# Kernel optimization log

Measured on AMD Instinct MI355X. Metric: run time of the kernel, lower is better.

Reference implementation:

```python
import jax, jax.numpy as jnp
import numpy as np

RES = 3.5
K = (np.pi / RES) ** 2          # Gaussian falloff constant
BW2 = 6.0                        # squared neighborhood radius (voxels)
R = 3                            # floor(idx - sqrt(6)) = idx-3, ceil(idx + sqrt(6)) = idx+3


def _offsets():
    o = jnp.arange(-R, R + 1)
    oz, oy, ox = jnp.meshgrid(o, o, o, indexing='ij')
    offs = jnp.stack([oz.ravel(), oy.ravel(), ox.ravel()], axis=-1)  # (343, 3)
    d2 = jnp.sum(offs * offs, axis=-1)                               # (343,)
    return offs, d2


def _splat(coords, x0, y0, z0, vox, G):
    """coords: (N,3) atom positions. Returns (G,G,G) density grid via scatter-max."""
    idx = jnp.stack([
        jnp.floor((coords[:, 0] - x0[0]) / vox[0]),
        jnp.floor((coords[:, 1] - y0[0]) / vox[0]),
        jnp.floor((coords[:, 2] - z0[0]) / vox[0]),
    ], axis=1).astype(jnp.int32)                                     # (N, 3)

    offs, d2 = _offsets()
    pos = idx[:, None, :] + offs[None, :, :]                         # (N, 343, 3)

    M = G - 1                                                        # min(dims) - 1 (cubic grid)
    lc = jnp.clip(idx - R, 0, M)                                     # clamped bbox lower (N,3)
    uc = jnp.clip(idx + R, 0, M)                                     # clamped bbox upper (N,3)
    in_range = jnp.all((pos >= lc[:, None, :]) & (pos <= uc[:, None, :]), axis=-1)
    center_ok = jnp.all((idx >= 0) & (idx < G), axis=-1)             # atom's own voxel inside grid
    valid = in_range & (d2 <= BW2)[None, :] & center_ok[:, None]     # (N, 343)

    prob = jnp.where(valid, jnp.exp(-K * d2.astype(jnp.float32))[None, :], 0.0)

    pos_c = jnp.clip(pos, 0, G - 1)                                  # safe indices for invalid slots
    flat = (pos_c[..., 0] * G + pos_c[..., 1]) * G + pos_c[..., 2]   # (N, 343)

    grid = jnp.zeros((G * G * G,), dtype=jnp.float32)
    grid = grid.at[flat.reshape(-1)].max(prob.reshape(-1))           # scatter-max (grid init 0, prob >= 0)
    return grid.reshape(G, G, G)


def setup_inputs() -> dict:
    key = jax.random.key(0)
    k1, k2 = jax.random.split(key)
    G = 256
    N = 20000
    src = jax.random.uniform(k1, (1, 3, N), dtype=jnp.float32, minval=0.0, maxval=float(G))
    tgt = jax.random.uniform(k2, (1, 3, N), dtype=jnp.float32, minval=0.0, maxval=float(G))
    return {
        'src': src,
        'tgt': tgt,
        'x_origin': jnp.zeros((1,), jnp.float32),
        'y_origin': jnp.zeros((1,), jnp.float32),
        'z_origin': jnp.zeros((1,), jnp.float32),
        'x_voxel': jnp.ones((1,), jnp.float32),
        'grid_dim': G,
    }


def reference(src, tgt, x_origin, y_origin, z_origin, x_voxel, grid_dim):
    G = int(grid_dim)
    src_c = src[0].T                                                 # (N, 3)
    tgt_c = tgt[0].T
    src_mask = _splat(src_c, x_origin, y_origin, z_origin, x_voxel, G)
    tgt_mask = _splat(tgt_c, x_origin, y_origin, z_origin, x_voxel, G)
    # global_alignment_loss: tgt <- tgt*src ; src <- src*src ; loss = mean(sum(src) - sum(tgt))
    rho_em = jnp.sum(tgt_mask * src_mask)
    rho_mo = jnp.sum(src_mask * src_mask)
    return rho_mo - rho_em
```

## Files before the change

### kernel.cpp

```cpp
#include <hip/hip_runtime.h>

#define GDIM   256
#define NCOLS  1024
#define CAP    128
#define NQ     2048

__global__ void bin_kernel(const float* __restrict__ src,
                           const float* __restrict__ tgt,
                           const float* __restrict__ ox,
                           const float* __restrict__ oy,
                           const float* __restrict__ oz,
                           const float* __restrict__ vox,
                           unsigned* __restrict__ cnt,
                           unsigned* __restrict__ entries,
                           float* __restrict__ out,
                           int N)
{
    int a = blockIdx.x * blockDim.x + threadIdx.x;
    int m = blockIdx.y;
    if (a == 0 && m == 0) *out = 0.0f;
    if (a >= N) return;

    const float* c = m ? tgt : src;
    float vx = vox[0];
    int i0 = (int)floorf((c[a]         - ox[0]) / vx);
    int i1 = (int)floorf((c[N + a]     - oy[0]) / vx);
    int i2 = (int)floorf((c[2 * N + a] - oz[0]) / vx);
    if ((unsigned)i0 >= GDIM || (unsigned)i1 >= GDIM || (unsigned)i2 >= GDIM) return;

    unsigned pk = (unsigned)i0 | ((unsigned)i1 << 8) | ((unsigned)i2 << 16);
    int tlx = max(i0 - 2, 0) >> 4, thx = min(i0 + 2, GDIM - 1) >> 4;
    int tly = max(i1 - 2, 0) >> 4, thy = min(i1 + 2, GDIM - 1) >> 4;
    int tlz = max(i2 - 2, 0) >> 6, thz = min(i2 + 2, GDIM - 1) >> 6;

    for (int tx = tlx; tx <= thx; ++tx)
        for (int ty = tly; ty <= thy; ++ty)
            for (int tz = tlz; tz <= thz; ++tz) {
                int bin = m * NCOLS + (((tx << 4) + ty) << 2) + tz;
                unsigned slot = atomicAdd(&cnt[bin], 1u);
                if (slot < CAP) entries[bin * CAP + slot] = pk;
            }
}

__global__ __launch_bounds__(256, 4)
void tile_kernel(const unsigned* __restrict__ cnt,
                 const unsigned* __restrict__ entries,
                 float* __restrict__ out)
{
    __shared__ unsigned long long smem[2 * NQ];
    __shared__ unsigned eS[CAP], eT[CAP];
    __shared__ float tblp[49];
    __shared__ float wsum[4];

    constexpr int OX[21] = {-2,-2,-2,-1,-1,-1,-1,-1, 0, 0, 0, 0, 0, 1, 1, 1, 1, 1, 2, 2, 2};
    constexpr int OY[21] = {-1, 0, 1,-2,-1, 0, 1, 2,-2,-1, 0, 1, 2,-2,-1, 0, 1, 2,-1, 0, 1};
    constexpr unsigned long long PATC[21] = {
        0x0040204000ull, 0x0020102000ull, 0x0040204000ull,
        0x0040204000ull, 0x4008040840ull, 0x2004020420ull, 0x4008040840ull, 0x0040204000ull,
        0x0020102000ull, 0x2004020420ull, 0x1002010210ull, 0x2004020420ull, 0x0020102000ull,
        0x0040204000ull, 0x4008040840ull, 0x2004020420ull, 0x4008040840ull, 0x0040204000ull,
        0x0040204000ull, 0x0020102000ull, 0x0040204000ull,
    };

    int tid = threadIdx.x;
    int t   = blockIdx.x;
    int cx0 = (t >> 6) << 4;
    int cy0 = ((t >> 2) & 15) << 4;
    int cz0 = (t & 3) << 6;

    const float kf = (float)((3.14159265358979323846 / 3.5) * (3.14159265358979323846 / 3.5));
    if (tid < 49) {
        int a = tid / 7, b = tid - 7 * a;
        tblp[tid] = expf(-kf * (float)a) * expf(-kf * (float)b);
    }
    {
        uint4* zp = (uint4*)smem;
        #pragma unroll
        for (int i = 0; i < 8; ++i) zp[tid + i * 256] = make_uint4(0u, 0u, 0u, 0u);
    }
    int nS = min(cnt[t],         (unsigned)CAP);
    int nT = min(cnt[NCOLS + t], (unsigned)CAP);
    if (tid < nS) eS[tid] = entries[t * CAP + tid];
    if (tid < nT) eT[tid] = entries[(NCOLS + t) * CAP + tid];
    __syncthreads();

#define SPLAT_R(r) {                                                              \
        int l0 = x0 + OX[r];                                                      \
        int l1 = y0 + OY[r];                                                      \
        if ((unsigned)l0 < 16u && (unsigned)l1 < 16u) {                           \
            unsigned long long pat = (PATC[r] >> (8 * drop)) & kmask;             \
            if (pat) {                                                            \
                unsigned long long* q = base + (((l0 << 10) | (l1 << 6) | zb) >> 3); \
                unsigned long long lo = pat << (8 * off);                         \
                if (lo) atomicOr(q, lo);                                          \
                if (spill) {                                                      \
                    unsigned long long hi = pat >> (8 * (8 - off));               \
                    if (hi) atomicOr(q + 1, hi);                                  \
                }                                                                 \
            }                                                                     \
        }                                                                         \
    }
    {
        int lane = tid & 63, wv = tid >> 6;
        int nTot = nS + nT;
        for (int e = lane; e < nTot; e += 64) {
            int m        = e >= nS;
            unsigned pk  = m ? eT[e - nS] : eS[e];
            int i0 = pk & 255, i1 = (pk >> 8) & 255, i2 = (pk >> 16) & 255;
            int zs   = max(i2 - 2, cz0), ze = min(i2 + 2, cz0 + 63);
            int drop = zs - (i2 - 2), keep = ze - zs + 1;
            int zb   = zs - cz0;
            int off  = zb & 7;
            unsigned long long kmask = (1ull << (8 * keep)) - 1ull;
            int x0 = i0 - cx0, y0 = i1 - cy0;
            unsigned long long* base = smem + m * NQ;
            bool spill = (off + keep) > 8;
            if (wv == 0) {
                SPLAT_R(0) SPLAT_R(1) SPLAT_R(2) SPLAT_R(3) SPLAT_R(4) SPLAT_R(5)
            } else if (wv == 1) {
                SPLAT_R(6) SPLAT_R(7) SPLAT_R(8) SPLAT_R(9) SPLAT_R(10) SPLAT_R(11)
            } else if (wv == 2) {
                SPLAT_R(12) SPLAT_R(13) SPLAT_R(14) SPLAT_R(15) SPLAT_R(16)
            } else {
                SPLAT_R(17) SPLAT_R(18) SPLAT_R(19) SPLAT_R(20)
            }
        }
    }
#undef SPLAT_R
    __syncthreads();

    const unsigned long long H  = 0x8080808080808080ull;
    const unsigned long long B1 = 0x0101010101010101ull;
    const unsigned long long K7 = 0x7f7f7f7f7f7f7f7full;
    const ulonglong2* sp = (const ulonglong2*)smem;
    const ulonglong2* tp = (const ulonglong2*)(smem + NQ);

    ulonglong2 sv[4], tw[4];
    #pragma unroll
    for (int i = 0; i < 4; ++i) {
        sv[i] = sp[tid + i * 256];
        tw[i] = tp[tid + i * 256];
    }

    int cd[7] = {0, 0, 0, 0, 0, 0, 0};
    float accC = 0.0f;
    #pragma unroll
    for (int i = 0; i < 4; ++i) {
        #pragma unroll
        for (int k = 0; k < 2; ++k) {
            unsigned long long w = k ? sv[i].y : sv[i].x;
            unsigned long long v = k ? tw[i].y : tw[i].x;
            unsigned long long q   = w | H;
            unsigned long long lsb = q & (~q + B1);
            #pragma unroll
            for (int d = 0; d < 7; ++d)
                cd[d] += __popcll(lsb & (B1 << d));
            unsigned long long bth = ((w + K7) & H) & ((v + K7) & H);
            while (bth) {
                int bit = __ffsll((long long)bth) - 1;
                int sh  = bit & ~7;
                int ds  = __ffs((int)((unsigned)(w >> sh) & 0x7fu)) - 1;
                int dt  = __ffs((int)((unsigned)(v >> sh) & 0x7fu)) - 1;
                accC += tblp[ds * 7 + dt];
                bth &= bth - 1;
            }
        }
    }
    float acc = -accC;
    #pragma unroll
    for (int d = 0; d < 7; ++d) {
        float tv = expf(-kf * (float)d);
        acc = fmaf((float)cd[d], tv * tv, acc);
    }

    #pragma unroll
    for (int off2 = 32; off2 > 0; off2 >>= 1)
        acc += __shfl_down(acc, off2, 64);
    int lane = tid & 63, wv = tid >> 6;
    if (lane == 0) wsum[wv] = acc;
    __syncthreads();
    if (tid == 0)
        atomicAdd(out, wsum[0] + wsum[1] + wsum[2] + wsum[3]);
}

extern "C" void kernel_launch(void* const* d_in, const int* in_sizes, int n_in,
                              void* d_out, int out_size, void* d_ws, size_t ws_size,
                              hipStream_t stream)
{
    const float* src = (const float*)d_in[0];
    const float* tgt = (const float*)d_in[1];
    const float* ox  = (const float*)d_in[2];
    const float* oy  = (const float*)d_in[3];
    const float* oz  = (const float*)d_in[4];
    const float* vox = (const float*)d_in[5];
    int N = in_sizes[0] / 3;

    unsigned* cnt     = (unsigned*)d_ws;
    unsigned* entries = cnt + 2 * NCOLS;

    hipMemsetAsync(cnt, 0, 2 * NCOLS * sizeof(unsigned), stream);

    dim3 bgrid((N + 255) / 256, 2);
    bin_kernel<<<bgrid, 256, 0, stream>>>(src, tgt, ox, oy, oz, vox, cnt, entries,
                                          (float*)d_out, N);
    tile_kernel<<<NCOLS, 256, 0, stream>>>(cnt, entries, (float*)d_out);
}
```

Baseline: 93.22 us.

## Spread final reduction over 64 partial slots with last-block ticket finalize

Each tile block now adds its sum into one of 64 partial accumulators instead of a single global float, and a ticket counter lets the last block reduce the partials and write the output. This is meant to cut contention on one atomic address and removes the output zeroing from the bin kernel. The entry buffers are merged into one shared array to drop a select, and the count loop skips zero source words. It adds a threadfence/ticket protocol and a larger memset.

```diff
diff --git a/kernel.cpp b/kernel.cpp
--- a/kernel.cpp
+++ b/kernel.cpp
@@ -4,6 +4,11 @@
 #define NCOLS  1024
 #define CAP    128
 #define NQ     2048
+
+#define WS_TICKET   2048
+#define WS_PARTIAL  2064
+#define WS_ENTRIES  2176
+#define WS_ZERO_B   (WS_ENTRIES * 4)
 
 __global__ void bin_kernel(const float* __restrict__ src,
                            const float* __restrict__ tgt,
@@ -13,12 +18,10 @@
                            const float* __restrict__ vox,
                            unsigned* __restrict__ cnt,
                            unsigned* __restrict__ entries,
-                           float* __restrict__ out,
                            int N)
 {
     int a = blockIdx.x * blockDim.x + threadIdx.x;
     int m = blockIdx.y;
-    if (a == 0 && m == 0) *out = 0.0f;
     if (a >= N) return;
 
     const float* c = m ? tgt : src;
@@ -45,12 +48,15 @@
 __global__ __launch_bounds__(256, 4)
 void tile_kernel(const unsigned* __restrict__ cnt,
                  const unsigned* __restrict__ entries,
+                 float* __restrict__ partials,
+                 unsigned* __restrict__ ticket,
                  float* __restrict__ out)
 {
     __shared__ unsigned long long smem[2 * NQ];
-    __shared__ unsigned eS[CAP], eT[CAP];
+    __shared__ unsigned eAll[2 * CAP];
     __shared__ float tblp[49];
     __shared__ float wsum[4];
+    __shared__ int   isLast;
 
     constexpr int OX[21] = {-2,-2,-2,-1,-1,-1,-1,-1, 0, 0, 0, 0, 0, 1, 1, 1, 1, 1, 2, 2, 2};
     constexpr int OY[21] = {-1, 0, 1,-2,-1, 0, 1, 2,-2,-1, 0, 1, 2,-2,-1, 0, 1, 2,-1, 0, 1};
@@ -80,8 +86,8 @@
     }
     int nS = min(cnt[t],         (unsigned)CAP);
     int nT = min(cnt[NCOLS + t], (unsigned)CAP);
-    if (tid < nS) eS[tid] = entries[t * CAP + tid];
-    if (tid < nT) eT[tid] = entries[(NCOLS + t) * CAP + tid];
+    if (tid < nS) eAll[tid]      = entries[t * CAP + tid];
+    if (tid < nT) eAll[nS + tid] = entries[(NCOLS + t) * CAP + tid];
     __syncthreads();
 
 #define SPLAT_R(r) {                                                              \
@@ -105,7 +111,7 @@
         int nTot = nS + nT;
         for (int e = lane; e < nTot; e += 64) {
             int m        = e >= nS;
-            unsigned pk  = m ? eT[e - nS] : eS[e];
+            unsigned pk  = eAll[e];
             int i0 = pk & 255, i1 = (pk >> 8) & 255, i2 = (pk >> 16) & 255;
             int zs   = max(i2 - 2, cz0), ze = min(i2 + 2, cz0 + 63);
             int drop = zs - (i2 - 2), keep = ze - zs + 1;
@@ -146,6 +152,7 @@
     float accC = 0.0f;
     #pragma unroll
     for (int i = 0; i < 4; ++i) {
+        if ((sv[i].x | sv[i].y) == 0ull) continue;
         #pragma unroll
         for (int k = 0; k < 2; ++k) {
             unsigned long long w = k ? sv[i].y : sv[i].x;
@@ -179,8 +186,24 @@
     int lane = tid & 63, wv = tid >> 6;
     if (lane == 0) wsum[wv] = acc;
     __syncthreads();
-    if (tid == 0)
-        atomicAdd(out, wsum[0] + wsum[1] + wsum[2] + wsum[3]);
+
+    if (tid == 0) {
+        float bs = wsum[0] + wsum[1] + wsum[2] + wsum[3];
+        atomicAdd(&partials[t & 63], bs);
+        __threadfence();
+        unsigned r = atomicAdd(ticket, 1u);
+        isLast = (r == NCOLS - 1);
+        __threadfence();
+    }
+    __syncthreads();
+    if (isLast && tid < 64) {
+        float v = __hip_atomic_load(&partials[tid], __ATOMIC_RELAXED,
+                                    __HIP_MEMORY_SCOPE_AGENT);
+        #pragma unroll
+        for (int o = 32; o > 0; o >>= 1)
+            v += __shfl_down(v, o, 64);
+        if (tid == 0) *out = v;
+    }
 }
 
 extern "C" void kernel_launch(void* const* d_in, const int* in_sizes, int n_in,
@@ -195,13 +218,15 @@
     const float* vox = (const float*)d_in[5];
     int N = in_sizes[0] / 3;
 
-    unsigned* cnt     = (unsigned*)d_ws;
-    unsigned* entries = cnt + 2 * NCOLS;
-
-    hipMemsetAsync(cnt, 0, 2 * NCOLS * sizeof(unsigned), stream);
+    unsigned* ws      = (unsigned*)d_ws;
+    unsigned* cnt     = ws;
+    unsigned* ticket  = ws + WS_TICKET;
+    float*    parts   = (float*)(ws + WS_PARTIAL);
+    unsigned* entries = ws + WS_ENTRIES;
+
+    hipMemsetAsync(ws, 0, WS_ZERO_B, stream);
 
     dim3 bgrid((N + 255) / 256, 2);
-    bin_kernel<<<bgrid, 256, 0, stream>>>(src, tgt, ox, oy, oz, vox, cnt, entries,
-                                          (float*)d_out, N);
-    tile_kernel<<<NCOLS, 256, 0, stream>>>(cnt, entries, (float*)d_out);
+    bin_kernel<<<bgrid, 256, 0, stream>>>(src, tgt, ox, oy, oz, vox, cnt, entries, N);
+    tile_kernel<<<NCOLS, 256, 0, stream>>>(cnt, entries, parts, ticket, (float*)d_out);
 }
```

Result: slower. 110.7 us (+18.7%).
